# Kernel tuning notes

Measured on AMD Instinct MI355X. Metric: run time of the kernel, lower is better.

The kernel has to match this reference:

```python
import jax, jax.numpy as jnp
import numpy as np

D_MODEL = 512
NUM_HEADS = 8
D_HEAD = D_MODEL // NUM_HEADS


def setup_inputs() -> dict:
    key = jax.random.key(0)
    ks = jax.random.split(key, 9)
    B, L = 4, 2048
    s = 1.0 / np.sqrt(D_MODEL)
    inp = {
        "x": jax.random.normal(ks[0], (B, L, D_MODEL), dtype=jnp.float32),
        "Wq": jax.random.uniform(ks[1], (D_MODEL, D_MODEL), jnp.float32, -s, s),
        "bq": jax.random.uniform(ks[2], (D_MODEL,), jnp.float32, -s, s),
        "Wk": jax.random.uniform(ks[3], (D_MODEL, D_MODEL), jnp.float32, -s, s),
        "bk": jax.random.uniform(ks[4], (D_MODEL,), jnp.float32, -s, s),
        "Wv": jax.random.uniform(ks[5], (D_MODEL, D_MODEL), jnp.float32, -s, s),
        "bv": jax.random.uniform(ks[6], (D_MODEL,), jnp.float32, -s, s),
        "Wo": jax.random.uniform(ks[7], (D_MODEL, D_MODEL), jnp.float32, -s, s),
        "bo": jax.random.uniform(ks[8], (D_MODEL,), jnp.float32, -s, s),
    }
    return inp


def reference(x, Wq, bq, Wk, bk, Wv, bv, Wo, bo):
    B, L, _ = x.shape
    def split_heads(t):  # [B,L,D] -> [B,H,L,d]
        return t.reshape(B, L, NUM_HEADS, D_HEAD).transpose(0, 2, 1, 3)
    Q = split_heads(x @ Wq + bq)
    K = split_heads(x @ Wk + bk)
    V = split_heads(x @ Wv + bv)
    scale = 1.0 / jnp.sqrt(jnp.asarray(D_HEAD, dtype=x.dtype))
    scores = jnp.einsum('bhqd,bhkd->bhqk', Q, K) * scale  # [B,H,L,L]
    weights = jax.nn.softmax(scores, axis=-1)
    z = jnp.einsum('bhqk,bhkd->bhqd', weights, V)  # [B,H,L,d]
    z = z.transpose(0, 2, 1, 3).reshape(B, L, D_MODEL)
    return z @ Wo + bo
```

## Files before the change

### kernel.cpp

```cpp
#include <hip/hip_runtime.h>
#include <hip/hip_bf16.h>
#include <math.h>


#define MDIM 8192
#define DMODEL 512
#define NHEAD 8
#define DHEAD 64
#define LSEQ 2048

typedef __attribute__((ext_vector_type(8))) short short8;
typedef __attribute__((ext_vector_type(4))) float floatx4;

struct alignas(16) bf16x8 { __hip_bfloat16 v[8]; };
struct alignas(8)  bf16x4 { __hip_bfloat16 v[4]; };

__device__ __forceinline__ void load_lds16(const __hip_bfloat16* g, __hip_bfloat16* l) {
    __builtin_amdgcn_global_load_lds(
        (const __attribute__((address_space(1))) void*)g,
        (__attribute__((address_space(3))) void*)l,
        16, 0, 0);
}

__device__ __forceinline__ float fast_exp2(float x) {
#if __has_builtin(__builtin_amdgcn_exp2f)
    return __builtin_amdgcn_exp2f(x);
#else
    return __expf(x * 0.69314718055994531f);
#endif
}

__global__ __launch_bounds__(256) void cast_x_kernel(
    const float* __restrict__ x, __hip_bfloat16* __restrict__ xb)
{
    size_t i = ((size_t)blockIdx.x * 256 + threadIdx.x) * 8;
    float4 a = *reinterpret_cast<const float4*>(x + i);
    float4 b = *reinterpret_cast<const float4*>(x + i + 4);
    bf16x8 o;
    o.v[0] = __float2bfloat16(a.x); o.v[1] = __float2bfloat16(a.y);
    o.v[2] = __float2bfloat16(a.z); o.v[3] = __float2bfloat16(a.w);
    o.v[4] = __float2bfloat16(b.x); o.v[5] = __float2bfloat16(b.y);
    o.v[6] = __float2bfloat16(b.z); o.v[7] = __float2bfloat16(b.w);
    *reinterpret_cast<bf16x8*>(xb + i) = o;
}

__global__ __launch_bounds__(256) void transpose_cast_w(
    const float* __restrict__ Wq, const float* __restrict__ Wk,
    const float* __restrict__ Wv, const float* __restrict__ Wo,
    __hip_bfloat16* __restrict__ Wt)
{
    __shared__ float t[32][33];
    const int z = blockIdx.z;
    const float* W = z == 0 ? Wq : (z == 1 ? Wk : (z == 2 ? Wv : Wo));
    __hip_bfloat16* dst = Wt + ((size_t)z << 18);
    int k0 = blockIdx.x * 32, n0 = blockIdx.y * 32;
    int c = threadIdx.x & 31, r = threadIdx.x >> 5;
    #pragma unroll
    for (int i = 0; i < 4; ++i)
        t[r + 8 * i][c] = W[(size_t)(k0 + r + 8 * i) * DMODEL + n0 + c];
    __syncthreads();
    #pragma unroll
    for (int i = 0; i < 4; ++i)
        dst[(size_t)(n0 + r + 8 * i) * DMODEL + k0 + c] = __float2bfloat16(t[c][r + 8 * i]);
}

__global__ __launch_bounds__(256) void gemm_qkv_mfma(
    const __hip_bfloat16* __restrict__ xb,
    const __hip_bfloat16* __restrict__ Wt,
    const float* __restrict__ bq, const float* __restrict__ bk,
    const float* __restrict__ bv,
    __hip_bfloat16* __restrict__ Q2, __hip_bfloat16* __restrict__ K2,
    __hip_bfloat16* __restrict__ V2)
{
    __shared__ __hip_bfloat16 As[128 * 64];
    __shared__ __hip_bfloat16 Bs[128 * 64];

    const int tid = threadIdx.x;
    const int wid = tid >> 6, lane = tid & 63;
    const int l16 = lane & 15, quad = lane >> 4;
    const int wr = wid >> 1, wc = wid & 1;
    const int row0 = blockIdx.x * 128;
    const int which = blockIdx.y >> 2;
    const int col0 = (blockIdx.y & 3) * 128;
    const __hip_bfloat16* Wb = Wt + ((size_t)which << 18);
    const float* bias = which == 0 ? bq : (which == 1 ? bk : bv);

    const int r8 = lane >> 3, slot = lane & 7;
    const int cchunk = slot ^ (r8 & 7);

    floatx4 acc[4][4];
    #pragma unroll
    for (int i = 0; i < 4; ++i)
        #pragma unroll
        for (int j = 0; j < 4; ++j) acc[i][j] = floatx4{0.f, 0.f, 0.f, 0.f};

    for (int kt = 0; kt < DMODEL / 64; ++kt) {
        __syncthreads();
        #pragma unroll
        for (int j = 0; j < 4; ++j) {
            int seg = wid * 4 + j;
            int m = seg * 8 + r8;
            load_lds16(xb + (size_t)(row0 + m) * DMODEL + kt * 64 + cchunk * 8,
                       As + seg * 512);
            load_lds16(Wb + (size_t)(col0 + m) * DMODEL + kt * 64 + cchunk * 8,
                       Bs + seg * 512);
        }
        __syncthreads();

        #pragma unroll
        for (int ks = 0; ks < 2; ++ks) {
            const int c = ks * 4 + quad;
            short8 af[4], bf[4];
            #pragma unroll
            for (int mt = 0; mt < 4; ++mt) {
                int m = wr * 64 + mt * 16 + l16;
                af[mt] = *reinterpret_cast<const short8*>(As + m * 64 + ((c ^ (m & 7)) << 3));
            }
            #pragma unroll
            for (int nt = 0; nt < 4; ++nt) {
                int n = wc * 64 + nt * 16 + l16;
                bf[nt] = *reinterpret_cast<const short8*>(Bs + n * 64 + ((c ^ (n & 7)) << 3));
            }
            if (which < 2) {
                #pragma unroll
                for (int mt = 0; mt < 4; ++mt)
                    #pragma unroll
                    for (int nt = 0; nt < 4; ++nt)
                        acc[mt][nt] = __builtin_amdgcn_mfma_f32_16x16x32_bf16(
                            bf[nt], af[mt], acc[mt][nt], 0, 0, 0);
            } else {
                #pragma unroll
                for (int mt = 0; mt < 4; ++mt)
                    #pragma unroll
                    for (int nt = 0; nt < 4; ++nt)
                        acc[mt][nt] = __builtin_amdgcn_mfma_f32_16x16x32_bf16(
                            af[mt], bf[nt], acc[mt][nt], 0, 0, 0);
            }
        }
    }

    const float QSCALE = 0.18033688011112042f;

    if (which < 2) {
        __hip_bfloat16* dst = (which == 0) ? Q2 : K2;
        const float sc = (which == 0) ? QSCALE : 1.0f;
        #pragma unroll
        for (int mt = 0; mt < 4; ++mt) {
            const int mm = row0 + wr * 64 + mt * 16 + l16;
            const int b = mm >> 11, l = mm & 2047;
            int rowi;
            if (which == 0) {
                rowi = l;
            } else {
                int hi = l & ~127, w7 = l & 127;
                rowi = hi | (w7 & 96) | (((w7 >> 3) & 3) << 2)
                          | (((w7 >> 2) & 1) << 4) | (w7 & 3);
            }
            #pragma unroll
            for (int nt = 0; nt < 4; ++nt) {
                const int nnb = col0 + wc * 64 + nt * 16 + quad * 4;
                const float4 bv4 = *reinterpret_cast<const float4*>(&bias[nnb]);
                const int h = nnb >> 6, d = nnb & 63;
                const int s = d >> 5, q4 = (d >> 3) & 3, jb = d & 7;
                bf16x4 pk;
                pk.v[0] = __float2bfloat16((acc[mt][nt][0] + bv4.x) * sc);
                pk.v[1] = __float2bfloat16((acc[mt][nt][1] + bv4.y) * sc);
                pk.v[2] = __float2bfloat16((acc[mt][nt][2] + bv4.z) * sc);
                pk.v[3] = __float2bfloat16((acc[mt][nt][3] + bv4.w) * sc);
                size_t idx = ((((size_t)(b * NHEAD + h) * 128 + (rowi >> 4)) * 2 + s) << 9)
                             + q4 * 128 + (rowi & 15) * 8 + jb;
                *reinterpret_cast<bf16x4*>(dst + idx) = pk;
            }
        }
    } else {
        #pragma unroll
        for (int mt = 0; mt < 4; ++mt) {
            const int mmb = row0 + wr * 64 + mt * 16 + quad * 4;
            const int b = mmb >> 11, lb = mmb & 2047;
            #pragma unroll
            for (int nt = 0; nt < 4; ++nt) {
                const int nn = col0 + wc * 64 + nt * 16 + l16;
                const int h = nn >> 6, d = nn & 63;
                const float bv = bias[nn];
                bf16x4 pk;
                pk.v[0] = __float2bfloat16(acc[mt][nt][0] + bv);
                pk.v[1] = __float2bfloat16(acc[mt][nt][1] + bv);
                pk.v[2] = __float2bfloat16(acc[mt][nt][2] + bv);
                pk.v[3] = __float2bfloat16(acc[mt][nt][3] + bv);
                size_t idx = ((((size_t)(b * NHEAD + h) * 64 + (lb >> 5)) * 4 + (d >> 4)) << 9)
                             + ((lb >> 3) & 3) * 128 + (d & 15) * 8 + (lb & 7);
                *reinterpret_cast<bf16x4*>(V2 + idx) = pk;
            }
        }
    }
}

__global__ __launch_bounds__(256) void gemm_out_mfma(
    const __hip_bfloat16* __restrict__ Zb,
    const __hip_bfloat16* __restrict__ WoT,
    const float* __restrict__ bo, float* __restrict__ out)
{
    __shared__ __hip_bfloat16 As[128 * 64];
    __shared__ __hip_bfloat16 Bs[64 * 64];

    const int tid = threadIdx.x;
    const int wid = tid >> 6, lane = tid & 63;
    const int l16 = lane & 15, quad = lane >> 4;
    const int row0 = blockIdx.x * 128;
    const int col0 = blockIdx.y * 64;
    const int r8 = lane >> 3, slot = lane & 7;
    const int cchunk = slot ^ (r8 & 7);

    floatx4 acc[2][4];
    #pragma unroll
    for (int i = 0; i < 2; ++i)
        #pragma unroll
        for (int j = 0; j < 4; ++j) acc[i][j] = floatx4{0.f, 0.f, 0.f, 0.f};

    for (int kt = 0; kt < DMODEL / 64; ++kt) {
        __syncthreads();
        #pragma unroll
        for (int j = 0; j < 4; ++j) {
            int seg = wid * 4 + j;
            int m = seg * 8 + r8;
            load_lds16(Zb + (size_t)(row0 + m) * DMODEL + kt * 64 + cchunk * 8,
                       As + seg * 512);
        }
        #pragma unroll
        for (int j = 0; j < 2; ++j) {
            int seg = wid * 2 + j;
            int n = seg * 8 + r8;
            load_lds16(WoT + (size_t)(col0 + n) * DMODEL + kt * 64 + cchunk * 8,
                       Bs + seg * 512);
        }
        __syncthreads();

        #pragma unroll
        for (int ks = 0; ks < 2; ++ks) {
            const int c = ks * 4 + quad;
            short8 af[2], bf[4];
            #pragma unroll
            for (int mt = 0; mt < 2; ++mt) {
                int m = wid * 32 + mt * 16 + l16;
                af[mt] = *reinterpret_cast<const short8*>(As + m * 64 + ((c ^ (m & 7)) << 3));
            }
            #pragma unroll
            for (int nt = 0; nt < 4; ++nt) {
                int n = nt * 16 + l16;
                bf[nt] = *reinterpret_cast<const short8*>(Bs + n * 64 + ((c ^ (n & 7)) << 3));
            }
            #pragma unroll
            for (int mt = 0; mt < 2; ++mt)
                #pragma unroll
                for (int nt = 0; nt < 4; ++nt)
                    acc[mt][nt] = __builtin_amdgcn_mfma_f32_16x16x32_bf16(
                        af[mt], bf[nt], acc[mt][nt], 0, 0, 0);
        }
    }

    #pragma unroll
    for (int mt = 0; mt < 2; ++mt) {
        const int mmbase = row0 + wid * 32 + mt * 16 + quad * 4;
        #pragma unroll
        for (int nt = 0; nt < 4; ++nt) {
            const int nn = col0 + nt * 16 + l16;
            const float bias_v = bo[nn];
            #pragma unroll
            for (int r = 0; r < 4; ++r)
                out[(size_t)(mmbase + r) * DMODEL + nn] = acc[mt][nt][r] + bias_v;
        }
    }
}

__global__ __launch_bounds__(256) void attn_mfma(
    const __hip_bfloat16* __restrict__ Q2,
    const __hip_bfloat16* __restrict__ K2,
    const __hip_bfloat16* __restrict__ V2,
    __hip_bfloat16* __restrict__ Z)
{
    __shared__ float smem[4608];
    float* Lred = smem;
    float* Ored = smem + 256;

    const int bh = (blockIdx.x & 7) * 4 + ((blockIdx.x >> 3) & 3);
    const int qt = blockIdx.x >> 5;
    const int q0 = qt * 64;
    const int tid = threadIdx.x;
    const int wid = tid >> 6, lane = tid & 63;
    const int l16 = lane & 15, quad = lane >> 4;

    const __hip_bfloat16* Kc = K2 + (((size_t)bh * 128 * 2) << 9);
    const __hip_bfloat16* Vc = V2 + (((size_t)bh * 64 * 4) << 9);

    short8 qb[4][2];
    #pragma unroll
    for (int nt = 0; nt < 4; ++nt)
        #pragma unroll
        for (int s = 0; s < 2; ++s)
            qb[nt][s] = *reinterpret_cast<const short8*>(
                Q2 + ((((size_t)bh * 128 + qt * 4 + nt) * 2 + s) << 9) + lane * 8);

    floatx4 acc[4][4];
    #pragma unroll
    for (int i = 0; i < 4; ++i)
        #pragma unroll
        for (int j = 0; j < 4; ++j) acc[i][j] = floatx4{0.f, 0.f, 0.f, 0.f};
    floatx4 accl[4];
    #pragma unroll
    for (int i = 0; i < 4; ++i) accl[i] = floatx4{0.f, 0.f, 0.f, 0.f};

    union { short8 s8; __hip_bfloat16 h[8]; } onesu;
    #pragma unroll
    for (int i = 0; i < 8; ++i) onesu.h[i] = __float2bfloat16(1.0f);
    const short8 ones = onesu.s8;

    const floatx4 fzero = floatx4{0.f, 0.f, 0.f, 0.f};

    const __hip_bfloat16* kp = Kc + (((size_t)wid * 4) << 9) + lane * 8;
    const __hip_bfloat16* vp = Vc + (((size_t)wid * 4) << 9) + lane * 8;

    for (int kt = 0; kt < LSEQ / 128; ++kt) {
        short8 kb[2][2], vb[4];
        #pragma unroll
        for (int t = 0; t < 2; ++t)
            #pragma unroll
            for (int s = 0; s < 2; ++s)
                kb[t][s] = *reinterpret_cast<const short8*>(kp + ((t * 2 + s) << 9));
        #pragma unroll
        for (int dt = 0; dt < 4; ++dt)
            vb[dt] = *reinterpret_cast<const short8*>(vp + (dt << 9));
        kp += (size_t)16 << 9;
        vp += (size_t)16 << 9;

        floatx4 sacc[2][4];
        #pragma unroll
        for (int nt = 0; nt < 4; ++nt) {
            sacc[0][nt] = __builtin_amdgcn_mfma_f32_16x16x32_bf16(
                kb[0][0], qb[nt][0], fzero, 0, 0, 0);
            sacc[1][nt] = __builtin_amdgcn_mfma_f32_16x16x32_bf16(
                kb[1][0], qb[nt][0], fzero, 0, 0, 0);
        }
        #pragma unroll
        for (int nt = 0; nt < 4; ++nt) {
            sacc[0][nt] = __builtin_amdgcn_mfma_f32_16x16x32_bf16(
                kb[0][1], qb[nt][1], sacc[0][nt], 0, 0, 0);
            sacc[1][nt] = __builtin_amdgcn_mfma_f32_16x16x32_bf16(
                kb[1][1], qb[nt][1], sacc[1][nt], 0, 0, 0);
        }

        short8 pa[4];
        #pragma unroll
        for (int nt = 0; nt < 4; ++nt) {
            union { short8 s8; __hip_bfloat16 h[8]; } u;
            #pragma unroll
            for (int t = 0; t < 2; ++t)
                #pragma unroll
                for (int r = 0; r < 4; ++r)
                    u.h[t * 4 + r] = __float2bfloat16(fast_exp2(sacc[t][nt][r]));
            pa[nt] = u.s8;
        }

        #pragma unroll
        for (int nt = 0; nt < 4; ++nt)
            accl[nt] = __builtin_amdgcn_mfma_f32_16x16x32_bf16(
                pa[nt], ones, accl[nt], 0, 0, 0);

        #pragma unroll
        for (int dt = 0; dt < 4; ++dt)
            #pragma unroll
            for (int nt = 0; nt < 4; ++nt)
                acc[nt][dt] = __builtin_amdgcn_mfma_f32_16x16x32_bf16(
                    pa[nt], vb[dt], acc[nt][dt], 0, 0, 0);
    }

    if (l16 == 0) {
        #pragma unroll
        for (int nt = 0; nt < 4; ++nt)
            #pragma unroll
            for (int r = 0; r < 4; ++r)
                Lred[wid * 64 + nt * 16 + quad * 4 + r] = accl[nt][r];
    }

    const int b = bh >> 3, h = bh & 7;
    const int ql = tid >> 2;
    const int dg = tid & 3;
    float inv = 0.f;

    for (int dt = 0; dt < 4; ++dt) {
        __syncthreads();
        #pragma unroll
        for (int nt = 0; nt < 4; ++nt)
            *reinterpret_cast<floatx4*>(
                &Ored[(wid * 16 + l16) * 68 + nt * 16 + quad * 4]) = acc[nt][dt];
        __syncthreads();

        if (dt == 0)
            inv = 1.f / (Lred[ql] + Lred[64 + ql] + Lred[128 + ql] + Lred[192 + ql]);

        bf16x4 zo;
        #pragma unroll
        for (int i = 0; i < 4; ++i) {
            int d = dg * 4 + i;
            float ssum = Ored[d * 68 + ql] + Ored[(16 + d) * 68 + ql]
                       + Ored[(32 + d) * 68 + ql] + Ored[(48 + d) * 68 + ql];
            zo.v[i] = __float2bfloat16(ssum * inv);
        }
        *reinterpret_cast<bf16x4*>(
            Z + (size_t)(b * LSEQ + q0 + ql) * DMODEL + h * 64 + dt * 16 + dg * 4) = zo;
    }
}

extern "C" void kernel_launch(void* const* d_in, const int* in_sizes, int n_in,
                              void* d_out, int out_size, void* d_ws, size_t ws_size,
                              hipStream_t stream)
{
    const float* x  = (const float*)d_in[0];
    const float* Wq = (const float*)d_in[1]; const float* bq = (const float*)d_in[2];
    const float* Wk = (const float*)d_in[3]; const float* bk = (const float*)d_in[4];
    const float* Wv = (const float*)d_in[5]; const float* bv = (const float*)d_in[6];
    const float* Wo = (const float*)d_in[7]; const float* bo = (const float*)d_in[8];
    float* out = (float*)d_out;

    const size_t nqkv = (size_t)MDIM * DMODEL;
    __hip_bfloat16* xb = (__hip_bfloat16*)d_ws;
    __hip_bfloat16* Wt = xb + nqkv;
    __hip_bfloat16* Q2 = Wt + ((size_t)4 << 18);
    __hip_bfloat16* K2 = Q2 + nqkv;
    __hip_bfloat16* V2 = K2 + nqkv;
    __hip_bfloat16* Zb = V2 + nqkv;

    cast_x_kernel<<<dim3(MDIM * DMODEL / (256 * 8)), 256, 0, stream>>>(x, xb);
    transpose_cast_w<<<dim3(16, 16, 4), 256, 0, stream>>>(Wq, Wk, Wv, Wo, Wt);

    gemm_qkv_mfma<<<dim3(MDIM / 128, 12), 256, 0, stream>>>(
        xb, Wt, bq, bk, bv, Q2, K2, V2);

    attn_mfma<<<dim3(32 * (LSEQ / 64)), 256, 0, stream>>>(Q2, K2, V2, Zb);

    gemm_out_mfma<<<dim3(MDIM / 128, DMODEL / 64), 256, 0, stream>>>(
        Zb, Wt + ((size_t)3 << 18), bo, out);
}
```

Before: 158.9 us.

## Software-pipeline K/V loads and QK MFMA; replace ones-MFMA row sum with shuffles

Result: no change. 158.0 us (-0.6%).

```diff
diff --git a/kernel.cpp b/kernel.cpp
--- a/kernel.cpp
+++ b/kernel.cpp
@@ -305,80 +305,106 @@
     for (int i = 0; i < 4; ++i)
         #pragma unroll
         for (int j = 0; j < 4; ++j) acc[i][j] = floatx4{0.f, 0.f, 0.f, 0.f};
-    floatx4 accl[4];
-    #pragma unroll
-    for (int i = 0; i < 4; ++i) accl[i] = floatx4{0.f, 0.f, 0.f, 0.f};
-
-    union { short8 s8; __hip_bfloat16 h[8]; } onesu;
-    #pragma unroll
-    for (int i = 0; i < 8; ++i) onesu.h[i] = __float2bfloat16(1.0f);
-    const short8 ones = onesu.s8;
+    float lsum[4] = {0.f, 0.f, 0.f, 0.f};
 
     const floatx4 fzero = floatx4{0.f, 0.f, 0.f, 0.f};
 
     const __hip_bfloat16* kp = Kc + (((size_t)wid * 4) << 9) + lane * 8;
     const __hip_bfloat16* vp = Vc + (((size_t)wid * 4) << 9) + lane * 8;
 
-    for (int kt = 0; kt < LSEQ / 128; ++kt) {
-        short8 kb[2][2], vb[4];
-        #pragma unroll
-        for (int t = 0; t < 2; ++t)
-            #pragma unroll
-            for (int s = 0; s < 2; ++s)
-                kb[t][s] = *reinterpret_cast<const short8*>(kp + ((t * 2 + s) << 9));
-        #pragma unroll
-        for (int dt = 0; dt < 4; ++dt)
-            vb[dt] = *reinterpret_cast<const short8*>(vp + (dt << 9));
-        kp += (size_t)16 << 9;
-        vp += (size_t)16 << 9;
-
-        floatx4 sacc[2][4];
+    short8 kb[2][2], vbuf[2][4];
+    #pragma unroll
+    for (int t = 0; t < 2; ++t)
+        #pragma unroll
+        for (int s = 0; s < 2; ++s)
+            kb[t][s] = *reinterpret_cast<const short8*>(kp + ((t * 2 + s) << 9));
+    #pragma unroll
+    for (int dt = 0; dt < 4; ++dt)
+        vbuf[0][dt] = *reinterpret_cast<const short8*>(vp + (dt << 9));
+    kp += (size_t)16 << 9;
+    vp += (size_t)16 << 9;
+
+    floatx4 sacc[2][4];
+    #pragma unroll
+    for (int nt = 0; nt < 4; ++nt) {
+        sacc[0][nt] = __builtin_amdgcn_mfma_f32_16x16x32_bf16(kb[0][0], qb[nt][0], fzero, 0, 0, 0);
+        sacc[1][nt] = __builtin_amdgcn_mfma_f32_16x16x32_bf16(kb[1][0], qb[nt][0], fzero, 0, 0, 0);
+    }
+    #pragma unroll
+    for (int nt = 0; nt < 4; ++nt) {
+        sacc[0][nt] = __builtin_amdgcn_mfma_f32_16x16x32_bf16(kb[0][1], qb[nt][1], sacc[0][nt], 0, 0, 0);
+        sacc[1][nt] = __builtin_amdgcn_mfma_f32_16x16x32_bf16(kb[1][1], qb[nt][1], sacc[1][nt], 0, 0, 0);
+    }
+
+    #pragma unroll
+    for (int kt = 0; kt < 16; ++kt) {
+        const int cur = kt & 1, nxt = cur ^ 1;
+
+        if (kt < 15) {
+            #pragma unroll
+            for (int t = 0; t < 2; ++t)
+                #pragma unroll
+                for (int s = 0; s < 2; ++s)
+                    kb[t][s] = *reinterpret_cast<const short8*>(kp + ((t * 2 + s) << 9));
+            #pragma unroll
+            for (int dt = 0; dt < 4; ++dt)
+                vbuf[nxt][dt] = *reinterpret_cast<const short8*>(vp + (dt << 9));
+            kp += (size_t)16 << 9;
+            vp += (size_t)16 << 9;
+        }
+
+        short8 pa[4];
         #pragma unroll
         for (int nt = 0; nt < 4; ++nt) {
-            sacc[0][nt] = __builtin_amdgcn_mfma_f32_16x16x32_bf16(
-                kb[0][0], qb[nt][0], fzero, 0, 0, 0);
-            sacc[1][nt] = __builtin_amdgcn_mfma_f32_16x16x32_bf16(
-                kb[1][0], qb[nt][0], fzero, 0, 0, 0);
-        }
-        #pragma unroll
-        for (int nt = 0; nt < 4; ++nt) {
-            sacc[0][nt] = __builtin_amdgcn_mfma_f32_16x16x32_bf16(
-                kb[0][1], qb[nt][1], sacc[0][nt], 0, 0, 0);
-            sacc[1][nt] = __builtin_amdgcn_mfma_f32_16x16x32_bf16(
-                kb[1][1], qb[nt][1], sacc[1][nt], 0, 0, 0);
-        }
-
-        short8 pa[4];
-        #pragma unroll
-        for (int nt = 0; nt < 4; ++nt) {
-            union { short8 s8; __hip_bfloat16 h[8]; } u;
+            float e[8];
             #pragma unroll
             for (int t = 0; t < 2; ++t)
                 #pragma unroll
                 for (int r = 0; r < 4; ++r)
-                    u.h[t * 4 + r] = __float2bfloat16(fast_exp2(sacc[t][nt][r]));
+                    e[t * 4 + r] = fast_exp2(sacc[t][nt][r]);
+            union { short8 s8; __hip_bfloat16 h[8]; } u;
+            #pragma unroll
+            for (int i = 0; i < 8; ++i) u.h[i] = __float2bfloat16(e[i]);
+            lsum[nt] += ((e[0] + e[1]) + (e[2] + e[3])) + ((e[4] + e[5]) + (e[6] + e[7]));
             pa[nt] = u.s8;
         }
 
-        #pragma unroll
-        for (int nt = 0; nt < 4; ++nt)
-            accl[nt] = __builtin_amdgcn_mfma_f32_16x16x32_bf16(
-                pa[nt], ones, accl[nt], 0, 0, 0);
+        if (kt < 15) {
+            #pragma unroll
+            for (int nt = 0; nt < 4; ++nt) {
+                sacc[0][nt] = __builtin_amdgcn_mfma_f32_16x16x32_bf16(
+                    kb[0][0], qb[nt][0], fzero, 0, 0, 0);
+                sacc[1][nt] = __builtin_amdgcn_mfma_f32_16x16x32_bf16(
+                    kb[1][0], qb[nt][0], fzero, 0, 0, 0);
+            }
+            #pragma unroll
+            for (int nt = 0; nt < 4; ++nt) {
+                sacc[0][nt] = __builtin_amdgcn_mfma_f32_16x16x32_bf16(
+                    kb[0][1], qb[nt][1], sacc[0][nt], 0, 0, 0);
+                sacc[1][nt] = __builtin_amdgcn_mfma_f32_16x16x32_bf16(
+                    kb[1][1], qb[nt][1], sacc[1][nt], 0, 0, 0);
+            }
+        }
 
         #pragma unroll
         for (int dt = 0; dt < 4; ++dt)
             #pragma unroll
             for (int nt = 0; nt < 4; ++nt)
                 acc[nt][dt] = __builtin_amdgcn_mfma_f32_16x16x32_bf16(
-                    pa[nt], vb[dt], acc[nt][dt], 0, 0, 0);
-    }
-
-    if (l16 == 0) {
+                    pa[nt], vbuf[cur][dt], acc[nt][dt], 0, 0, 0);
+    }
+
+    #pragma unroll
+    for (int nt = 0; nt < 4; ++nt) {
+        float v = lsum[nt];
+        v += __shfl_xor(v, 16);
+        v += __shfl_xor(v, 32);
+        lsum[nt] = v;
+    }
+    if (quad == 0) {
         #pragma unroll
         for (int nt = 0; nt < 4; ++nt)
-            #pragma unroll
-            for (int r = 0; r < 4; ++r)
-                Lred[wid * 64 + nt * 16 + quad * 4 + r] = accl[nt][r];
+            Lred[wid * 64 + nt * 16 + l16] = lsum[nt];
     }
 
     const int b = bh >> 3, h = bh & 7;
```
